# Optimization experiments

Hardware: AMD Instinct MI355X
Metric: run time of the kernel (lower is better)

Reference implementation:

```python
import jax, jax.numpy as jnp
import numpy as np

T = 500        # num_target
R = 50         # num_resource
NS = 1000      # hard-coded sample count in the torch loop
F_STATE = 2    # raw state features; num_feature = F_STATE + T = 502
NOISE_F = 2
H1, H2 = 32, 16
NEG_SLOPE = 0.2


def _lrelu(x):
    return jnp.where(x >= 0, x, NEG_SLOPE * x)


def setup_inputs() -> dict:
    key = jax.random.key(0)
    ks = jax.random.split(key, 16)
    d = {}
    d["state"] = jax.random.normal(ks[0], (1, T, F_STATE), jnp.float32)
    d["def_cur_loc"] = jax.random.uniform(ks[1], (R, T), jnp.float32)
    d["feat_noise"] = jax.random.uniform(ks[2], (1, T, NOISE_F), jnp.float32)
    d["gumbel_u"] = jax.random.uniform(ks[3], (NS, R, T), jnp.float32, 1e-6, 1.0 - 1e-6)
    # learned / fixed parameters
    d["payoff"] = jax.random.normal(ks[4], (T, T), jnp.float32)
    # row-normalized adjacency surrogate
    a = jax.random.uniform(ks[5], (T, T), jnp.float32)
    d["norm_adj"] = a / jnp.sum(a, axis=1, keepdims=True)
    fin = F_STATE + T + NOISE_F  # 504 = num_feature + noise_feat
    d["gc1_w"] = jax.random.normal(ks[6], (fin, H1), jnp.float32) / np.sqrt(fin)
    d["gc1_b"] = jnp.zeros((H1,), jnp.float32)
    d["gc2_w"] = jax.random.normal(ks[7], (H1, H2), jnp.float32) / np.sqrt(H1)
    d["gc2_b"] = jnp.zeros((H2,), jnp.float32)
    d["bn_gamma"] = jnp.ones((T,), jnp.float32)
    d["bn_beta"] = jnp.zeros((T,), jnp.float32)
    d["actgen_w"] = jax.random.normal(ks[8], (H2 * T, T), jnp.float32) / np.sqrt(H2 * T)
    d["actgen_v"] = jax.random.normal(ks[9], (T, T), jnp.float32) / np.sqrt(T)
    return d


def reference(state, def_cur_loc, feat_noise, gumbel_u, payoff, norm_adj,
              gc1_w, gc1_b, gc2_w, gc2_b, bn_gamma, bn_beta,
              actgen_w, actgen_v):
    # x = cat(state, payoff, noise) -> (1, T, 504)
    x = jnp.concatenate([state, payoff[None], feat_noise], axis=2)

    def gcn(h, w, b):  # GraphConvolution: norm_adj @ (h @ w) + b
        return jnp.einsum('tu,buc->btc', norm_adj, h @ w) + b

    def bn(h):  # BatchNorm1d(T) in eval mode (running mean 0, var 1)
        return h * bn_gamma[None, :, None] + bn_beta[None, :, None]

    h = _lrelu(bn(gcn(x, gc1_w, gc1_b)))          # (1, T, 32); dropout is eval-mode identity
    h = _lrelu(bn(gcn(h, gc2_w, gc2_b)))          # (1, T, 16)
    xf = h.reshape(H2 * T)                        # x.view(-1, 16*T).squeeze()

    # act_gen: shared linear head + location projection -> per-resource logits (R, T)
    logits = xf @ actgen_w + def_cur_loc @ actgen_v

    # 1000 independent stochastic samples (the torch for-loop, fully batched):
    g = -jnp.log(-jnp.log(gumbel_u))              # (NS, R, T) gumbel noise
    act_estimates = jax.nn.softmax(logits[None] + g, axis=-1)  # (1000, R, T)
    # state_value head exists in the module but is not returned; omitted.
    return act_estimates
```

## Files before the change

kernel.cpp:

```cpp
#include <hip/hip_runtime.h>

#define T_ 500
#define R_ 50
#define NS_ 1000
#define H1_ 32
#define H2_ 16
#define NEG_ 0.2f
#define NROWS_ (NS_ * R_)

__device__ __forceinline__ float lrelu(float x) { return x >= 0.f ? x : NEG_ * x; }

__device__ __forceinline__ float wave_sum_dpp(float x) {
    int t;
    t = __builtin_amdgcn_update_dpp(0, __float_as_int(x), 0x111, 0xf, 0xf, true);
    x += __int_as_float(t);
    t = __builtin_amdgcn_update_dpp(0, __float_as_int(x), 0x112, 0xf, 0xf, true);
    x += __int_as_float(t);
    t = __builtin_amdgcn_update_dpp(0, __float_as_int(x), 0x114, 0xf, 0xf, true);
    x += __int_as_float(t);
    t = __builtin_amdgcn_update_dpp(0, __float_as_int(x), 0x118, 0xf, 0xf, true);
    x += __int_as_float(t);
    t = __builtin_amdgcn_update_dpp(0, __float_as_int(x), 0x142, 0xf, 0xf, true);
    x += __int_as_float(t);
    t = __builtin_amdgcn_update_dpp(0, __float_as_int(x), 0x143, 0xf, 0xf, true);
    x += __int_as_float(t);
    return __int_as_float(__builtin_amdgcn_readlane(__float_as_int(x), 63));
}

__global__ __launch_bounds__(256) void k1_xw(const float* __restrict__ state,
                                             const float* __restrict__ payoff,
                                             const float* __restrict__ noise,
                                             const float* __restrict__ w,
                                             float* __restrict__ y1) {
    __shared__ float xs[504];
    __shared__ float red[8][H1_];
    int t = blockIdx.x, tid = threadIdx.x;
    for (int u = tid; u < T_; u += 256) xs[2 + u] = payoff[t * T_ + u];
    if (tid == 0) {
        xs[0] = state[t * 2];     xs[1] = state[t * 2 + 1];
        xs[502] = noise[t * 2];   xs[503] = noise[t * 2 + 1];
    }
    __syncthreads();
    int c = tid & 31, kg = tid >> 5;
    float acc = 0.f;
#pragma unroll 7
    for (int f = kg; f < 504; f += 8) acc += xs[f] * w[f * H1_ + c];
    red[kg][c] = acc;
    __syncthreads();
    if (tid < H1_) {
        float a = 0.f;
#pragma unroll
        for (int s = 0; s < 8; ++s) a += red[s][tid];
        y1[t * H1_ + tid] = a;
    }
}

__global__ __launch_bounds__(256) void k2_adj_fused(const float* __restrict__ adj,
                                                    const float* __restrict__ y1,
                                                    const float* __restrict__ b,
                                                    const float* __restrict__ gamma,
                                                    const float* __restrict__ beta,
                                                    const float* __restrict__ w2,
                                                    float* __restrict__ y2) {
    __shared__ float arow[T_];
    __shared__ float red[8][H1_];
    __shared__ float h1row[H1_];
    int t = blockIdx.x, tid = threadIdx.x;
    for (int u = tid; u < T_; u += 256) arow[u] = adj[t * T_ + u];
    __syncthreads();
    int c = tid & 31, kg = tid >> 5;
    float acc = 0.f;
#pragma unroll 4
    for (int u = kg; u < T_; u += 8) acc += arow[u] * y1[u * H1_ + c];
    red[kg][c] = acc;
    __syncthreads();
    if (tid < H1_) {
        float a = 0.f;
#pragma unroll
        for (int s = 0; s < 8; ++s) a += red[s][tid];
        h1row[tid] = lrelu((a + b[tid]) * gamma[t] + beta[t]);
    }
    __syncthreads();
    if (tid < H2_) {
        float a = 0.f;
#pragma unroll
        for (int cc = 0; cc < H1_; ++cc) a += h1row[cc] * w2[cc * H2_ + tid];
        y2[t * H2_ + tid] = a;
    }
}

__global__ __launch_bounds__(256) void k3_adj2_aw(const float* __restrict__ adj,
                                                  const float* __restrict__ y2,
                                                  const float* __restrict__ b2,
                                                  const float* __restrict__ gamma,
                                                  const float* __restrict__ beta,
                                                  const float* __restrict__ aw,
                                                  float* __restrict__ part1) {
    __shared__ float arow[T_];
    __shared__ float red[16][H2_];
    __shared__ float xfr[H2_];
    int t = blockIdx.x, tid = threadIdx.x;
    for (int u = tid; u < T_; u += 256) arow[u] = adj[t * T_ + u];
    __syncthreads();
    int c2 = tid & 15, kg = tid >> 4;
    float acc = 0.f;
#pragma unroll 4
    for (int u = kg; u < T_; u += 16) acc += arow[u] * y2[u * H2_ + c2];
    red[kg][c2] = acc;
    __syncthreads();
    if (tid < H2_) {
        float a = 0.f;
#pragma unroll
        for (int s = 0; s < 16; ++s) a += red[s][tid];
        xfr[tid] = lrelu((a + b2[tid]) * gamma[t] + beta[t]);
    }
    __syncthreads();
    float acc0 = 0.f, acc1 = 0.f;
#pragma unroll
    for (int c = 0; c < H2_; ++c) {
        float xv = xfr[c];
        const float* awr = aw + (t * H2_ + c) * T_;
        acc0 += xv * awr[tid];
        if (tid < T_ - 256) acc1 += xv * awr[256 + tid];
    }
    part1[t * T_ + tid] = acc0;
    if (tid < T_ - 256) part1[t * T_ + 256 + tid] = acc1;
}

__global__ __launch_bounds__(256) void k4_logits_part(const float* __restrict__ dloc,
                                                      const float* __restrict__ av,
                                                      const float* __restrict__ part1,
                                                      float* __restrict__ part2) {
    int r = blockIdx.x;
    int jb = blockIdx.y & 1, q = blockIdx.y >> 1;
    __shared__ float drow[125];
    int tid = threadIdx.x;
    int t0 = q * 125;
    if (tid < 125) drow[tid] = dloc[r * T_ + t0 + tid];
    __syncthreads();
    if (tid >= 250) return;
    int j = jb * 250 + tid;
    float acc = 0.f;
#pragma unroll 5
    for (int i = 0; i < 125; ++i) {
        int t = t0 + i;
        acc += drow[i] * av[t * T_ + j] + part1[t * T_ + j];
    }
    part2[q * (R_ * T_) + r * T_ + j] = acc;
}

__global__ __launch_bounds__(256) void k4_reduce_exp(const float* __restrict__ part2,
                                                     float* __restrict__ elog) {
    int gid = blockIdx.x * 256 + threadIdx.x;
    if (gid >= R_ * T_) return;
    float v = part2[gid] + part2[R_ * T_ + gid] +
              part2[2 * R_ * T_ + gid] + part2[3 * R_ * T_ + gid];
    elog[gid] = __expf(v);
}

__global__ __launch_bounds__(256) void k7_softmax(const float4* __restrict__ gu,
                                                  const float4* __restrict__ elog,
                                                  float4* __restrict__ out) {
    __shared__ float4 esm[125];
    int b = blockIdx.x;
    int sg = b / R_;
    int r  = b - sg * R_;
    int tid = threadIdx.x;
    if (tid < 125) esm[tid] = elog[r * 125 + tid];
    __syncthreads();

    int wave = tid >> 6, lane = tid & 63;
    int row = (sg * 4 + wave) * R_ + r;
    bool has1 = lane < 61;

    const float4* grow = gu + (size_t)row * 125;
    float4 g0 = grow[lane];
    float4 g1;
    if (has1) g1 = grow[64 + lane];
    float4 e0 = esm[lane];
    float4 e1 = has1 ? esm[64 + lane] : e0;

    float p[8];
    p[0] = e0.x * __builtin_amdgcn_rcpf(-__log2f(g0.x));
    p[1] = e0.y * __builtin_amdgcn_rcpf(-__log2f(g0.y));
    p[2] = e0.z * __builtin_amdgcn_rcpf(-__log2f(g0.z));
    p[3] = e0.w * __builtin_amdgcn_rcpf(-__log2f(g0.w));
    if (has1) {
        p[4] = e1.x * __builtin_amdgcn_rcpf(-__log2f(g1.x));
        p[5] = e1.y * __builtin_amdgcn_rcpf(-__log2f(g1.y));
        p[6] = e1.z * __builtin_amdgcn_rcpf(-__log2f(g1.z));
        p[7] = e1.w * __builtin_amdgcn_rcpf(-__log2f(g1.w));
    } else {
        p[4] = p[5] = p[6] = p[7] = 0.f;
    }
    float s = ((p[0] + p[1]) + (p[2] + p[3])) + ((p[4] + p[5]) + (p[6] + p[7]));
    float tot = wave_sum_dpp(s);
    float inv = __builtin_amdgcn_rcpf(tot);

    float4* orow = out + (size_t)row * 125;
    float4 o0 = {p[0] * inv, p[1] * inv, p[2] * inv, p[3] * inv};
    orow[lane] = o0;
    if (has1) {
        float4 o1 = {p[4] * inv, p[5] * inv, p[6] * inv, p[7] * inv};
        orow[64 + lane] = o1;
    }
}

extern "C" void kernel_launch(void* const* d_in, const int* in_sizes, int n_in,
                              void* d_out, int out_size, void* d_ws, size_t ws_size,
                              hipStream_t stream) {
    const float* state  = (const float*)d_in[0];
    const float* dloc   = (const float*)d_in[1];
    const float* noise  = (const float*)d_in[2];
    const float* gu     = (const float*)d_in[3];
    const float* payoff = (const float*)d_in[4];
    const float* adj    = (const float*)d_in[5];
    const float* g1w    = (const float*)d_in[6];
    const float* g1b    = (const float*)d_in[7];
    const float* g2w    = (const float*)d_in[8];
    const float* g2b    = (const float*)d_in[9];
    const float* gamma  = (const float*)d_in[10];
    const float* beta   = (const float*)d_in[11];
    const float* aw     = (const float*)d_in[12];
    const float* av     = (const float*)d_in[13];
    float* out = (float*)d_out;

    float* ws     = (float*)d_ws;
    float* y1     = ws;
    float* y2     = ws + 16000;
    float* part1  = ws + 24000;
    float* part2  = ws + 274000;
    float* elog   = ws + 374000;

    k1_xw<<<T_, 256, 0, stream>>>(state, payoff, noise, g1w, y1);
    k2_adj_fused<<<T_, 256, 0, stream>>>(adj, y1, g1b, gamma, beta, g2w, y2);
    k3_adj2_aw<<<T_, 256, 0, stream>>>(adj, y2, g2b, gamma, beta, aw, part1);
    k4_logits_part<<<dim3(R_, 8), 256, 0, stream>>>(dloc, av, part1, part2);
    k4_reduce_exp<<<(R_ * T_ + 255) / 256, 256, 0, stream>>>(part2, elog);
    k7_softmax<<<NROWS_ / 4, 256, 0, stream>>>(
        (const float4*)gu, (const float4*)elog, (float4*)out);
}
```

Before: 73.50 us.

## Stage gumbel rows via global_load_lds and process four rows per wave

The softmax kernel now has each wave handle four contiguous rows instead of one. All four rows' gumbel inputs are issued up front as direct global-to-LDS loads, followed by a single wait. The per-resource exp(logits) vector is read straight from global memory for each row instead of being staged in shared memory. The aim is more memory-level parallelism per wave and fewer blocks, but it adds LDS pressure (32 KB per block), which lowers occupancy and relies on the asynchronous LDS load path.

```diff
diff --git a/kernel.cpp b/kernel.cpp
--- a/kernel.cpp
+++ b/kernel.cpp
@@ -7,6 +7,7 @@
 #define H2_ 16
 #define NEG_ 0.2f
 #define NROWS_ (NS_ * R_)
+#define TROWS_ 16
 
 __device__ __forceinline__ float lrelu(float x) { return x >= 0.f ? x : NEG_ * x; }
 
@@ -158,51 +159,64 @@
     elog[gid] = __expf(v);
 }
 
-__global__ __launch_bounds__(256) void k7_softmax(const float4* __restrict__ gu,
+typedef const char __attribute__((address_space(1)))* gas_p;
+typedef char __attribute__((address_space(3)))* las_p;
+
+__global__ __launch_bounds__(256) void k7_softmax(const float* __restrict__ gu,
                                                   const float4* __restrict__ elog,
                                                   float4* __restrict__ out) {
-    __shared__ float4 esm[125];
+    __shared__ char sm[TROWS_ * 2000];
     int b = blockIdx.x;
-    int sg = b / R_;
-    int r  = b - sg * R_;
     int tid = threadIdx.x;
-    if (tid < 125) esm[tid] = elog[r * 125 + tid];
-    __syncthreads();
-
     int wave = tid >> 6, lane = tid & 63;
-    int row = (sg * 4 + wave) * R_ + r;
+    int rbase = b * TROWS_ + wave * 4;
     bool has1 = lane < 61;
 
-    const float4* grow = gu + (size_t)row * 125;
-    float4 g0 = grow[lane];
-    float4 g1;
-    if (has1) g1 = grow[64 + lane];
-    float4 e0 = esm[lane];
-    float4 e1 = has1 ? esm[64 + lane] : e0;
-
-    float p[8];
-    p[0] = e0.x * __builtin_amdgcn_rcpf(-__log2f(g0.x));
-    p[1] = e0.y * __builtin_amdgcn_rcpf(-__log2f(g0.y));
-    p[2] = e0.z * __builtin_amdgcn_rcpf(-__log2f(g0.z));
-    p[3] = e0.w * __builtin_amdgcn_rcpf(-__log2f(g0.w));
-    if (has1) {
-        p[4] = e1.x * __builtin_amdgcn_rcpf(-__log2f(g1.x));
-        p[5] = e1.y * __builtin_amdgcn_rcpf(-__log2f(g1.y));
-        p[6] = e1.z * __builtin_amdgcn_rcpf(-__log2f(g1.z));
-        p[7] = e1.w * __builtin_amdgcn_rcpf(-__log2f(g1.w));
-    } else {
-        p[4] = p[5] = p[6] = p[7] = 0.f;
-    }
-    float s = ((p[0] + p[1]) + (p[2] + p[3])) + ((p[4] + p[5]) + (p[6] + p[7]));
-    float tot = wave_sum_dpp(s);
-    float inv = __builtin_amdgcn_rcpf(tot);
-
-    float4* orow = out + (size_t)row * 125;
-    float4 o0 = {p[0] * inv, p[1] * inv, p[2] * inv, p[3] * inv};
-    orow[lane] = o0;
-    if (has1) {
-        float4 o1 = {p[4] * inv, p[5] * inv, p[6] * inv, p[7] * inv};
-        orow[64 + lane] = o1;
+    const char* gbase = (const char*)gu;
+#pragma unroll
+    for (int j = 0; j < 4; ++j) {
+        size_t goff = (size_t)(rbase + j) * 2000;
+        int loff = (wave * 4 + j) * 2000;
+        __builtin_amdgcn_global_load_lds((gas_p)(gbase + goff) + lane * 16,
+                                         (las_p)(sm + loff), 16, 0, 0);
+        if (has1)
+            __builtin_amdgcn_global_load_lds((gas_p)(gbase + goff + 1024) + lane * 16,
+                                             (las_p)(sm + loff + 1024), 16, 0, 0);
+    }
+    asm volatile("s_waitcnt vmcnt(0)" ::: "memory");
+
+#pragma unroll
+    for (int j = 0; j < 4; ++j) {
+        int row = rbase + j;
+        const float4* lrow = (const float4*)(sm + (wave * 4 + j) * 2000);
+        float4 g0 = lrow[lane];
+        float4 g1 = has1 ? lrow[64 + lane] : g0;
+        const float4* ep = elog + (row % R_) * 125;
+        float4 e0 = ep[lane];
+        float4 e1 = has1 ? ep[64 + lane] : e0;
+
+        float p0 = e0.x * __builtin_amdgcn_rcpf(-__log2f(g0.x));
+        float p1 = e0.y * __builtin_amdgcn_rcpf(-__log2f(g0.y));
+        float p2 = e0.z * __builtin_amdgcn_rcpf(-__log2f(g0.z));
+        float p3 = e0.w * __builtin_amdgcn_rcpf(-__log2f(g0.w));
+        float p4 = 0.f, p5 = 0.f, p6 = 0.f, p7 = 0.f;
+        if (has1) {
+            p4 = e1.x * __builtin_amdgcn_rcpf(-__log2f(g1.x));
+            p5 = e1.y * __builtin_amdgcn_rcpf(-__log2f(g1.y));
+            p6 = e1.z * __builtin_amdgcn_rcpf(-__log2f(g1.z));
+            p7 = e1.w * __builtin_amdgcn_rcpf(-__log2f(g1.w));
+        }
+        float s = ((p0 + p1) + (p2 + p3)) + ((p4 + p5) + (p6 + p7));
+        float tot = wave_sum_dpp(s);
+        float inv = __builtin_amdgcn_rcpf(tot);
+
+        float4* orow = out + (size_t)row * 125;
+        float4 o0 = {p0 * inv, p1 * inv, p2 * inv, p3 * inv};
+        orow[lane] = o0;
+        if (has1) {
+            float4 o1 = {p4 * inv, p5 * inv, p6 * inv, p7 * inv};
+            orow[64 + lane] = o1;
+        }
     }
 }
 
@@ -237,6 +251,6 @@
     k3_adj2_aw<<<T_, 256, 0, stream>>>(adj, y2, g2b, gamma, beta, aw, part1);
     k4_logits_part<<<dim3(R_, 8), 256, 0, stream>>>(dloc, av, part1, part2);
     k4_reduce_exp<<<(R_ * T_ + 255) / 256, 256, 0, stream>>>(part2, elog);
-    k7_softmax<<<NROWS_ / 4, 256, 0, stream>>>(
-        (const float4*)gu, (const float4*)elog, (float4*)out);
-}
+    k7_softmax<<<NROWS_ / TROWS_, 256, 0, stream>>>(
+        gu, (const float4*)elog, (float4*)out);
+}
```

Measured after the change: 78.70 us. 1.07x slower.

## Double-buffer gumbel rows into LDS via async global_load_lds in softmax kernel

Applied to the files above, without the earlier changes.

The softmax kernel now gives each wave eight sample rows for one resource, not a single row. Rows are staged into per-wave LDS buffers with asynchronous global-to-LDS loads and double-buffered using explicit vmcnt waits, so loads of later rows overlap compute and stores of earlier ones. The per-resource exp-logit vector is loaded once per wave into registers, and the block-level shared copy and barrier are dropped. In exchange the grid is much smaller, each block uses 32KB of LDS, which caps occupancy, and correctness depends on hand-counted vmcnt values that also count stores.

```diff
diff --git a/kernel.cpp b/kernel.cpp
--- a/kernel.cpp
+++ b/kernel.cpp
@@ -7,6 +7,7 @@
 #define H2_ 16
 #define NEG_ 0.2f
 #define NROWS_ (NS_ * R_)
+#define NSLOT_ 6250
 
 __device__ __forceinline__ float lrelu(float x) { return x >= 0.f ? x : NEG_ * x; }
 
@@ -158,52 +159,92 @@
     elog[gid] = __expf(v);
 }
 
-__global__ __launch_bounds__(256) void k7_softmax(const float4* __restrict__ gu,
+typedef const char __attribute__((address_space(1)))* gas_p;
+typedef char __attribute__((address_space(3)))* las_p;
+
+__global__ __launch_bounds__(256) void k7_softmax(const float* __restrict__ gu,
                                                   const float4* __restrict__ elog,
                                                   float4* __restrict__ out) {
-    __shared__ float4 esm[125];
-    int b = blockIdx.x;
-    int sg = b / R_;
-    int r  = b - sg * R_;
+    __shared__ char sm[4][2][2][2000];
     int tid = threadIdx.x;
-    if (tid < 125) esm[tid] = elog[r * 125 + tid];
-    __syncthreads();
-
     int wave = tid >> 6, lane = tid & 63;
-    int row = (sg * 4 + wave) * R_ + r;
+    int slot = blockIdx.x * 4 + wave;
+    if (slot >= NSLOT_) return;
+    int r = slot % R_;
+    int chunk = slot / R_;
+    int q0 = chunk * 8;
     bool has1 = lane < 61;
-
-    const float4* grow = gu + (size_t)row * 125;
-    float4 g0 = grow[lane];
-    float4 g1;
-    if (has1) g1 = grow[64 + lane];
-    float4 e0 = esm[lane];
-    float4 e1 = has1 ? esm[64 + lane] : e0;
-
-    float p[8];
-    p[0] = e0.x * __builtin_amdgcn_rcpf(-__log2f(g0.x));
-    p[1] = e0.y * __builtin_amdgcn_rcpf(-__log2f(g0.y));
-    p[2] = e0.z * __builtin_amdgcn_rcpf(-__log2f(g0.z));
-    p[3] = e0.w * __builtin_amdgcn_rcpf(-__log2f(g0.w));
-    if (has1) {
-        p[4] = e1.x * __builtin_amdgcn_rcpf(-__log2f(g1.x));
-        p[5] = e1.y * __builtin_amdgcn_rcpf(-__log2f(g1.y));
-        p[6] = e1.z * __builtin_amdgcn_rcpf(-__log2f(g1.z));
-        p[7] = e1.w * __builtin_amdgcn_rcpf(-__log2f(g1.w));
-    } else {
-        p[4] = p[5] = p[6] = p[7] = 0.f;
-    }
-    float s = ((p[0] + p[1]) + (p[2] + p[3])) + ((p[4] + p[5]) + (p[6] + p[7]));
-    float tot = wave_sum_dpp(s);
-    float inv = __builtin_amdgcn_rcpf(tot);
-
-    float4* orow = out + (size_t)row * 125;
-    float4 o0 = {p[0] * inv, p[1] * inv, p[2] * inv, p[3] * inv};
-    orow[lane] = o0;
-    if (has1) {
-        float4 o1 = {p[4] * inv, p[5] * inv, p[6] * inv, p[7] * inv};
-        orow[64 + lane] = o1;
-    }
+    int iA = lane, iB = has1 ? 64 + lane : lane;
+
+    const float4* ep = elog + r * 125;
+    float4 e0 = ep[iA];
+    float4 e1 = ep[iB];
+
+    const char* gbase = (const char*)gu;
+    char* smw = &sm[wave][0][0][0];
+
+#define STAGE(BUF, G)                                                          \
+    do {                                                                       \
+        _Pragma("unroll")                                                      \
+        for (int k = 0; k < 2; ++k) {                                          \
+            int q = q0 + 2 * (G) + k;                                          \
+            size_t goff = ((size_t)q * R_ + r) * 2000;                         \
+            char* l = smw + ((BUF) * 2 + k) * 2000;                            \
+            __builtin_amdgcn_global_load_lds((gas_p)(gbase + goff) + lane * 16,\
+                                             (las_p)l, 16, 0, 0);              \
+            if (has1)                                                          \
+                __builtin_amdgcn_global_load_lds(                              \
+                    (gas_p)(gbase + goff + 1024) + lane * 16,                  \
+                    (las_p)(l + 1024), 16, 0, 0);                              \
+        }                                                                      \
+    } while (0)
+
+#define PROC(BUF, G)                                                           \
+    do {                                                                       \
+        _Pragma("unroll")                                                      \
+        for (int k = 0; k < 2; ++k) {                                          \
+            int q = q0 + 2 * (G) + k;                                          \
+            const float4* lrow = (const float4*)(smw + ((BUF) * 2 + k) * 2000);\
+            float4 g0 = lrow[iA];                                              \
+            float4 g1 = lrow[iB];                                              \
+            float p0 = e0.x * __builtin_amdgcn_rcpf(-__log2f(g0.x));           \
+            float p1 = e0.y * __builtin_amdgcn_rcpf(-__log2f(g0.y));           \
+            float p2 = e0.z * __builtin_amdgcn_rcpf(-__log2f(g0.z));           \
+            float p3 = e0.w * __builtin_amdgcn_rcpf(-__log2f(g0.w));           \
+            float p4 = 0.f, p5 = 0.f, p6 = 0.f, p7 = 0.f;                      \
+            if (has1) {                                                        \
+                p4 = e1.x * __builtin_amdgcn_rcpf(-__log2f(g1.x));             \
+                p5 = e1.y * __builtin_amdgcn_rcpf(-__log2f(g1.y));             \
+                p6 = e1.z * __builtin_amdgcn_rcpf(-__log2f(g1.z));             \
+                p7 = e1.w * __builtin_amdgcn_rcpf(-__log2f(g1.w));             \
+            }                                                                  \
+            float s = ((p0 + p1) + (p2 + p3)) + ((p4 + p5) + (p6 + p7));       \
+            float tot = wave_sum_dpp(s);                                       \
+            float inv = __builtin_amdgcn_rcpf(tot);                            \
+            float4* orow = out + ((size_t)q * R_ + r) * 125;                   \
+            float4 o0 = {p0 * inv, p1 * inv, p2 * inv, p3 * inv};              \
+            orow[iA] = o0;                                                     \
+            if (has1) {                                                        \
+                float4 o1 = {p4 * inv, p5 * inv, p6 * inv, p7 * inv};          \
+                orow[64 + lane] = o1;                                          \
+            }                                                                  \
+        }                                                                      \
+    } while (0)
+
+    STAGE(0, 0);
+    STAGE(1, 1);
+    asm volatile("s_waitcnt vmcnt(4)" ::: "memory");
+    PROC(0, 0);
+    STAGE(0, 2);
+    asm volatile("s_waitcnt vmcnt(8)" ::: "memory");
+    PROC(1, 1);
+    STAGE(1, 3);
+    asm volatile("s_waitcnt vmcnt(8)" ::: "memory");
+    PROC(0, 2);
+    asm volatile("s_waitcnt vmcnt(4)" ::: "memory");
+    PROC(1, 3);
+#undef STAGE
+#undef PROC
 }
 
 extern "C" void kernel_launch(void* const* d_in, const int* in_sizes, int n_in,
@@ -237,6 +278,6 @@
     k3_adj2_aw<<<T_, 256, 0, stream>>>(adj, y2, g2b, gamma, beta, aw, part1);
     k4_logits_part<<<dim3(R_, 8), 256, 0, stream>>>(dloc, av, part1, part2);
     k4_reduce_exp<<<(R_ * T_ + 255) / 256, 256, 0, stream>>>(part2, elog);
-    k7_softmax<<<NROWS_ / 4, 256, 0, stream>>>(
-        (const float4*)gu, (const float4*)elog, (float4*)out);
-}
+    k7_softmax<<<(NSLOT_ + 3) / 4, 256, 0, stream>>>(
+        gu, (const float4*)elog, (float4*)out);
+}
```

Result: no change. 73.97 us (+0.6%).
